# Optimization experiments

Hardware: AMD Instinct MI355X
Metric: run time of the kernel (lower is better)

Reference implementation:

```python
import jax, jax.numpy as jnp
import numpy as np

B, T, D, H = 4, 4096, 2048, 128

def setup_inputs() -> dict:
    key = jax.random.key(0)
    k1, k2, k3, k4 = jax.random.split(key, 4)
    scale = 0.02
    return {
        "x": jax.random.normal(k1, (B, T, D), dtype=jnp.float32),
        "Wq": jax.random.normal(k2, (D, H), dtype=jnp.float32) * scale,
        "Wk": jax.random.normal(k3, (D, H), dtype=jnp.float32) * scale,
        "Wv": jax.random.normal(k4, (D, H), dtype=jnp.float32) * scale,
    }

def reference(x, Wq, Wk, Wv):
    # x: [B,T,D]; projections to [B,T,H]
    q = jnp.einsum('btd,dh->bth', x, Wq)
    k = jnp.einsum('btd,dh->bth', x, Wk)
    v = jnp.einsum('btd,dh->bth', x, Wv)
    scale = 1.0 / jnp.sqrt(jnp.asarray(q.shape[-1], q.dtype))
    scores = jnp.einsum('bth,bsh->bts', q, k) * scale  # [B,T,T]
    t = x.shape[1]
    causal = jnp.tril(jnp.ones((t, t), dtype=bool))
    scores = jnp.where(causal, scores, -jnp.inf)
    weights = jax.nn.softmax(scores, axis=-1)
    # dropout p=0.0 (eval) -> identity
    out = jnp.einsum('bts,bsh->bth', weights, v)
    return out
```

## Files before the change

### kernel.cpp

```cpp
#include <hip/hip_runtime.h>
#include <hip/hip_bf16.h>

#define Bq 4
#define Tq 4096
#define Dq 2048
#define Hq 128
#define Mq (Bq*Tq)
#define CHUNK 16

typedef __attribute__((ext_vector_type(8))) short bf16x8;
typedef __attribute__((ext_vector_type(4))) float f32x4;

static __device__ __forceinline__ short bfbits(float f) {
    union { __hip_bfloat16 h; short s; } u;
    u.h = __float2bfloat16(f);
    return u.s;
}
static __device__ __forceinline__ float bf2f(short s) {
    union { unsigned u; float f; } v;
    v.u = ((unsigned)(unsigned short)s) << 16;
    return v.f;
}

__global__ __launch_bounds__(256, 1) void wt_kernel(
    const float* __restrict__ Wqp,
    const float* __restrict__ Wkp,
    const float* __restrict__ Wvp,
    short* __restrict__ wTg)
{
    __shared__ short trsp[128][136];
    const int kc = blockIdx.x;
    const int w  = blockIdx.y;
    const float* __restrict__ W = (w == 0) ? Wqp : (w == 1) ? Wkp : Wvp;
    const float scale = (w == 0) ? 0.08838834764831843f : 1.0f;
    const int t = threadIdx.x;

    #pragma unroll
    for (int i = 0; i < 16; i++) {
        int idx = t + i * 256;
        int r = idx >> 5, c4 = idx & 31;
        float4 f = *(const float4*)&W[(size_t)(kc * 128 + r) * Hq + c4 * 4];
        trsp[c4 * 4 + 0][r] = bfbits(f.x * scale);
        trsp[c4 * 4 + 1][r] = bfbits(f.y * scale);
        trsp[c4 * 4 + 2][r] = bfbits(f.z * scale);
        trsp[c4 * 4 + 3][r] = bfbits(f.w * scale);
    }
    __syncthreads();
    #pragma unroll
    for (int i = 0; i < 8; i++) {
        int idx = t + i * 256;
        int h = idx >> 4, c8 = idx & 15;
        *(bf16x8*)&wTg[((size_t)w * 128 + h) * Dq + kc * 128 + c8 * 8] =
            *(bf16x8*)&trsp[h][c8 * 8];
    }
}

__global__ __launch_bounds__(256, 1) void qkv_fused_kernel(
    const float* __restrict__ x,
    const short* __restrict__ wTg,
    short* __restrict__ qg,
    short* __restrict__ kg,
    short* __restrict__ vTt)
{
    __shared__ short smem[64 * 72 + 384 * 72];
    short (*xs)[72]  = (short(*)[72])smem;
    short (*wts)[72] = (short(*)[72])(smem + 64 * 72);

    const int m0 = blockIdx.x * 64;

    const int t    = threadIdx.x;
    const int lane = t & 63;
    const int qw   = t >> 6;
    const int l15  = lane & 15;
    const int quad = lane >> 4;

    f32x4 o[4][6];
    #pragma unroll
    for (int mf = 0; mf < 4; mf++)
        #pragma unroll
        for (int j = 0; j < 6; j++) o[mf][j] = (f32x4){0.f, 0.f, 0.f, 0.f};

    const int xr = t >> 2, xc = (t & 3) * 16;

    float4 xreg[4];
    bf16x8 wreg[12];
    {
        const float* src = x + (size_t)(m0 + xr) * Dq + xc;
        #pragma unroll
        for (int i = 0; i < 4; i++) xreg[i] = *(const float4*)(src + i * 4);
        #pragma unroll
        for (int i = 0; i < 12; i++) {
            int idx = t + i * 256;
            wreg[i] = *(const bf16x8*)&wTg[(size_t)(idx >> 3) * Dq + (idx & 7) * 8];
        }
    }

    for (int k0 = 0; k0 < Dq; k0 += 64) {
        __syncthreads();
        {
            bf16x8 v0, v1;
            v0[0] = bfbits(xreg[0].x); v0[1] = bfbits(xreg[0].y);
            v0[2] = bfbits(xreg[0].z); v0[3] = bfbits(xreg[0].w);
            v0[4] = bfbits(xreg[1].x); v0[5] = bfbits(xreg[1].y);
            v0[6] = bfbits(xreg[1].z); v0[7] = bfbits(xreg[1].w);
            v1[0] = bfbits(xreg[2].x); v1[1] = bfbits(xreg[2].y);
            v1[2] = bfbits(xreg[2].z); v1[3] = bfbits(xreg[2].w);
            v1[4] = bfbits(xreg[3].x); v1[5] = bfbits(xreg[3].y);
            v1[6] = bfbits(xreg[3].z); v1[7] = bfbits(xreg[3].w);
            *(bf16x8*)&xs[xr][xc]     = v0;
            *(bf16x8*)&xs[xr][xc + 8] = v1;
            #pragma unroll
            for (int i = 0; i < 12; i++) {
                int idx = t + i * 256;
                *(bf16x8*)&wts[idx >> 3][(idx & 7) * 8] = wreg[i];
            }
        }
        if (k0 + 64 < Dq) {
            const float* src = x + (size_t)(m0 + xr) * Dq + k0 + 64 + xc;
            #pragma unroll
            for (int i = 0; i < 4; i++) xreg[i] = *(const float4*)(src + i * 4);
            #pragma unroll
            for (int i = 0; i < 12; i++) {
                int idx = t + i * 256;
                wreg[i] = *(const bf16x8*)&wTg[(size_t)(idx >> 3) * Dq + k0 + 64 + (idx & 7) * 8];
            }
        }
        __syncthreads();

        #pragma unroll
        for (int kk = 0; kk < 2; kk++) {
            bf16x8 a[4], b[6];
            #pragma unroll
            for (int mf = 0; mf < 4; mf++)
                a[mf] = *(bf16x8*)&xs[mf * 16 + l15][kk * 32 + quad * 8];
            #pragma unroll
            for (int j = 0; j < 6; j++)
                b[j] = *(bf16x8*)&wts[(qw * 6 + j) * 16 + l15][kk * 32 + quad * 8];
            #pragma unroll
            for (int mf = 0; mf < 4; mf++)
                #pragma unroll
                for (int j = 0; j < 6; j++)
                    o[mf][j] = __builtin_amdgcn_mfma_f32_16x16x32_bf16(
                        a[mf], b[j], o[mf][j], 0, 0, 0);
        }
    }

    __syncthreads();
    {
        short (*e64)[264] = (short(*)[264])smem;
        #pragma unroll
        for (int mf = 0; mf < 4; mf++)
            #pragma unroll
            for (int j = 0; j < 6; j++) {
                int n0 = (qw * 6 + j) * 16;
                if (n0 < 256) {
                    #pragma unroll
                    for (int reg = 0; reg < 4; reg++)
                        e64[mf * 16 + quad * 4 + reg][n0 + l15] = bfbits(o[mf][j][reg]);
                }
            }
        __syncthreads();
        #pragma unroll
        for (int i = 0; i < 8; i++) {
            int idx = t + i * 256;
            int r = idx >> 5, u = idx & 31;
            int n = u * 8;
            bf16x8 val = *(bf16x8*)&e64[r][n];
            short* dst = (n < 128) ? &qg[(size_t)(m0 + r) * Hq + n]
                                   : &kg[(size_t)(m0 + r) * Hq + (n - 128)];
            *(bf16x8*)dst = val;
        }
    }
    __syncthreads();
    {
        short (*e128)[72] = (short(*)[72])smem;
        #pragma unroll
        for (int mf = 0; mf < 4; mf++)
            #pragma unroll
            for (int j = 0; j < 6; j++) {
                int n0 = (qw * 6 + j) * 16;
                if (n0 >= 256) {
                    short4 pk;
                    pk.x = bfbits(o[mf][j][0]); pk.y = bfbits(o[mf][j][1]);
                    pk.z = bfbits(o[mf][j][2]); pk.w = bfbits(o[mf][j][3]);
                    *(short4*)&e128[(n0 - 256) + l15][mf * 16 + quad * 4] = pk;
                }
            }
        __syncthreads();
        const int bb = m0 / Tq;
        const int jt = (m0 % Tq) >> 6;
        #pragma unroll
        for (int i = 0; i < 4; i++) {
            int idx = t + i * 256;
            int h = idx >> 3, u = idx & 7;
            *(bf16x8*)&vTt[(((size_t)bb * (Tq / 64) + jt) * 128 + h) * 64 + u * 8] =
                *(bf16x8*)&e128[h][u * 8];
        }
    }
}

__global__ __launch_bounds__(256, 2) void attn_part_kernel(
    const short* __restrict__ qg, const short* __restrict__ kg,
    const short* __restrict__ vTt,
    short* __restrict__ Opart,
    float2* __restrict__ ml)
{
    __shared__ short qs[64][136];
    __shared__ short ks[64][136];
    __shared__ short vt[128][72];
    __shared__ short ps[64][72];

    const int qt = blockIdx.x;
    const int b  = blockIdx.y;
    const int c  = blockIdx.z;
    const int q0 = qt * 64;

    const int lo = c * CHUNK;
    const int hi = min(qt + 1, lo + CHUNK);
    if (lo >= hi) return;

    const int t    = threadIdx.x;
    const int lane = t & 63;
    const int qw   = t >> 6;
    const int l15  = lane & 15;
    const int quad = lane >> 4;

    const size_t zoff = (size_t)c * Mq;

    #pragma unroll
    for (int i = 0; i < 4; i++) {
        int idx = t + i * 256;
        int r = idx >> 4, cc = idx & 15;
        *(bf16x8*)&qs[r][cc * 8] =
            *(const bf16x8*)&qg[(size_t)(b * Tq + q0 + r) * Hq + cc * 8];
    }

    float mcur[4], lrow[4];
    #pragma unroll
    for (int r = 0; r < 4; r++) { mcur[r] = -1e30f; lrow[r] = 0.f; }
    f32x4 o[8];
    #pragma unroll
    for (int nf = 0; nf < 8; nf++) o[nf] = (f32x4){0.f, 0.f, 0.f, 0.f};

    bf16x8 kreg[4], vreg[4];
    {
        const size_t kbase = (size_t)(b * Tq + lo * 64) * Hq;
        const short* vsrc = vTt + (((size_t)b * (Tq / 64) + lo) * 128) * 64;
        #pragma unroll
        for (int i = 0; i < 4; i++) {
            int idx = t + i * 256;
            kreg[i] = *(const bf16x8*)&kg[kbase + (size_t)(idx >> 4) * Hq + (idx & 15) * 8];
            vreg[i] = *(const bf16x8*)&vsrc[idx * 8];
        }
    }

    for (int jt = lo; jt < hi; jt++) {
        __syncthreads();

        #pragma unroll
        for (int i = 0; i < 4; i++) {
            int idx = t + i * 256;
            *(bf16x8*)&ks[idx >> 4][(idx & 15) * 8] = kreg[i];
            *(bf16x8*)&vt[idx >> 3][(idx & 7) * 8]  = vreg[i];
        }
        if (jt + 1 < hi) {
            const size_t kbase = (size_t)(b * Tq + (jt + 1) * 64) * Hq;
            const short* vsrc = vTt + (((size_t)b * (Tq / 64) + jt + 1) * 128) * 64;
            #pragma unroll
            for (int i = 0; i < 4; i++) {
                int idx = t + i * 256;
                kreg[i] = *(const bf16x8*)&kg[kbase + (size_t)(idx >> 4) * Hq + (idx & 15) * 8];
                vreg[i] = *(const bf16x8*)&vsrc[idx * 8];
            }
        }
        __syncthreads();

        f32x4 sacc[4];
        #pragma unroll
        for (int nf = 0; nf < 4; nf++) sacc[nf] = (f32x4){0.f, 0.f, 0.f, 0.f};
        #pragma unroll
        for (int kk = 0; kk < 4; kk++) {
            bf16x8 aq = *(bf16x8*)&qs[qw * 16 + l15][kk * 32 + quad * 8];
            #pragma unroll
            for (int nf = 0; nf < 4; nf++) {
                bf16x8 bk = *(bf16x8*)&ks[nf * 16 + l15][kk * 32 + quad * 8];
                sacc[nf] = __builtin_amdgcn_mfma_f32_16x16x32_bf16(aq, bk, sacc[nf], 0, 0, 0);
            }
        }

        const bool diag = (jt == qt);
        #pragma unroll
        for (int reg = 0; reg < 4; reg++) {
            const int rloc = qw * 16 + quad * 4 + reg;
            if (diag) {
                #pragma unroll
                for (int nf = 0; nf < 4; nf++)
                    if (nf * 16 + l15 > rloc) sacc[nf][reg] = -1e30f;
            }
            float m_r = fmaxf(fmaxf(sacc[0][reg], sacc[1][reg]),
                              fmaxf(sacc[2][reg], sacc[3][reg]));
            #pragma unroll
            for (int mm = 8; mm >= 1; mm >>= 1)
                m_r = fmaxf(m_r, __shfl_xor(m_r, mm, 16));
            float mnew  = fmaxf(mcur[reg], m_r);
            float alpha = __expf(mcur[reg] - mnew);
            mcur[reg]   = mnew;
            float rs = 0.f;
            #pragma unroll
            for (int nf = 0; nf < 4; nf++) {
                float p = __expf(sacc[nf][reg] - mnew);
                rs += p;
                ps[rloc][nf * 16 + l15] = bfbits(p);
            }
            #pragma unroll
            for (int mm = 8; mm >= 1; mm >>= 1)
                rs += __shfl_xor(rs, mm, 16);
            lrow[reg] = lrow[reg] * alpha + rs;
            #pragma unroll
            for (int nf = 0; nf < 8; nf++) o[nf][reg] *= alpha;
        }
        __threadfence_block();

        #pragma unroll
        for (int ks2 = 0; ks2 < 2; ks2++) {
            bf16x8 ap = *(bf16x8*)&ps[qw * 16 + l15][ks2 * 32 + quad * 8];
            #pragma unroll
            for (int nf = 0; nf < 8; nf++) {
                bf16x8 bv = *(bf16x8*)&vt[nf * 16 + l15][ks2 * 32 + quad * 8];
                o[nf] = __builtin_amdgcn_mfma_f32_16x16x32_bf16(ap, bv, o[nf], 0, 0, 0);
            }
        }
    }

    __syncthreads();
    #pragma unroll
    for (int nf = 0; nf < 8; nf++)
        #pragma unroll
        for (int reg = 0; reg < 4; reg++)
            ks[qw * 16 + quad * 4 + reg][nf * 16 + l15] = bfbits(o[nf][reg]);
    if (l15 == 0) {
        #pragma unroll
        for (int reg = 0; reg < 4; reg++)
            ml[zoff + (size_t)b * Tq + q0 + qw * 16 + quad * 4 + reg] =
                make_float2(mcur[reg], lrow[reg]);
    }
    __syncthreads();
    #pragma unroll
    for (int i = 0; i < 4; i++) {
        int idx = t + i * 256;
        int r = idx >> 4, cc = idx & 15;
        *(bf16x8*)&Opart[(zoff + (size_t)b * Tq + q0 + r) * Hq + cc * 8] =
            *(bf16x8*)&ks[r][cc * 8];
    }
}

__global__ __launch_bounds__(256, 4) void merge_kernel(
    const short* __restrict__ Opart, const float2* __restrict__ ml,
    float* __restrict__ outg)
{
    const int t   = threadIdx.x;
    const int row = blockIdx.x * 16 + (t >> 4);
    const int cu  = t & 15;

    const int rl  = row & (Tq - 1);
    const int nch = (rl >> 10) + 1;

    float m = ml[row].x;
    for (int cc = 1; cc < nch; cc++) m = fmaxf(m, ml[(size_t)cc * Mq + row].x);

    float lsum = 0.f;
    float acc[8] = {};
    for (int cc = 0; cc < nch; cc++) {
        float2 p = ml[(size_t)cc * Mq + row];
        float a = __expf(p.x - m);
        lsum += a * p.y;
        bf16x8 oc = *(const bf16x8*)&Opart[((size_t)cc * Mq + row) * Hq + cu * 8];
        #pragma unroll
        for (int j = 0; j < 8; j++) acc[j] += a * bf2f(oc[j]);
    }
    float inv = 1.0f / lsum;

    float4 r0, r1;
    r0.x = acc[0] * inv; r0.y = acc[1] * inv; r0.z = acc[2] * inv; r0.w = acc[3] * inv;
    r1.x = acc[4] * inv; r1.y = acc[5] * inv; r1.z = acc[6] * inv; r1.w = acc[7] * inv;
    float* dst = &outg[(size_t)row * Hq + cu * 8];
    *(float4*)dst       = r0;
    *(float4*)(dst + 4) = r1;
}

extern "C" void kernel_launch(void* const* d_in, const int* in_sizes, int n_in,
                              void* d_out, int out_size, void* d_ws, size_t ws_size,
                              hipStream_t stream) {
    const float* x   = (const float*)d_in[0];
    const float* Wqp = (const float*)d_in[1];
    const float* Wkp = (const float*)d_in[2];
    const float* Wvp = (const float*)d_in[3];
    float* out = (float*)d_out;

    short* qg    = (short*)d_ws;
    short* kg    = qg  + (size_t)Mq * Hq;
    short* vTt   = kg  + (size_t)Mq * Hq;
    short* Opart = vTt + (size_t)Mq * Hq;
    short* wTg   = Opart;
    float2* ml   = (float2*)(Opart + (size_t)4 * Mq * Hq);

    wt_kernel<<<dim3(16, 3), dim3(256), 0, stream>>>(Wqp, Wkp, Wvp, wTg);
    qkv_fused_kernel<<<dim3(Mq / 64), dim3(256), 0, stream>>>(x, wTg, qg, kg, vTt);
    attn_part_kernel<<<dim3(Tq / 64, Bq, 4), dim3(256), 0, stream>>>(qg, kg, vTt, Opart, ml);
    merge_kernel<<<dim3(Mq / 16), dim3(256), 0, stream>>>(Opart, ml, out);
}
```

Baseline: 319.1 us.

## Load K and V MFMA operands directly from global, drop LDS staging and barriers

The attention kernel no longer stages K and V tiles through shared memory with a register prefetch and two block barriers per key tile. Each wave now loads its MFMA B-operands straight from global memory (relying on L1/L2 since all four waves read the same tile). Shared memory shrinks to Q and P, so occupancy is raised from 2 to 4 blocks per CU. The trade-off is that K and V are fetched once per wave instead of once per block, the explicit prefetch of the next tile is gone, and global load latency now sits directly in front of the MFMAs.

```diff
diff --git a/kernel.cpp b/kernel.cpp
--- a/kernel.cpp
+++ b/kernel.cpp
@@ -199,16 +199,15 @@
     }
 }
 
-__global__ __launch_bounds__(256, 2) void attn_part_kernel(
+__global__ __launch_bounds__(256, 4) void attn_part_kernel(
     const short* __restrict__ qg, const short* __restrict__ kg,
     const short* __restrict__ vTt,
     short* __restrict__ Opart,
     float2* __restrict__ ml)
 {
-    __shared__ short qs[64][136];
-    __shared__ short ks[64][136];
-    __shared__ short vt[128][72];
-    __shared__ short ps[64][72];
+    __shared__ short smem[64 * 136 + 64 * 72];
+    short (*qs)[136] = (short(*)[136])smem;
+    short (*ps)[72]  = (short(*)[72])(smem + 64 * 136);
 
     const int qt = blockIdx.x;
     const int b  = blockIdx.y;
@@ -225,12 +224,10 @@
     const int l15  = lane & 15;
     const int quad = lane >> 4;
 
-    const size_t zoff = (size_t)c * Mq;
-
     #pragma unroll
     for (int i = 0; i < 4; i++) {
-        int idx = t + i * 256;
-        int r = idx >> 4, cc = idx & 15;
+        int idx = lane + i * 64;
+        int r = qw * 16 + (idx >> 4), cc = idx & 15;
         *(bf16x8*)&qs[r][cc * 8] =
             *(const bf16x8*)&qg[(size_t)(b * Tq + q0 + r) * Hq + cc * 8];
     }
@@ -242,50 +239,26 @@
     #pragma unroll
     for (int nf = 0; nf < 8; nf++) o[nf] = (f32x4){0.f, 0.f, 0.f, 0.f};
 
-    bf16x8 kreg[4], vreg[4];
-    {
-        const size_t kbase = (size_t)(b * Tq + lo * 64) * Hq;
-        const short* vsrc = vTt + (((size_t)b * (Tq / 64) + lo) * 128) * 64;
-        #pragma unroll
-        for (int i = 0; i < 4; i++) {
-            int idx = t + i * 256;
-            kreg[i] = *(const bf16x8*)&kg[kbase + (size_t)(idx >> 4) * Hq + (idx & 15) * 8];
-            vreg[i] = *(const bf16x8*)&vsrc[idx * 8];
-        }
-    }
+    const short* kptr = kg  + ((size_t)b * Tq + l15) * Hq + quad * 8;
+    const short* vptr = vTt + ((size_t)b * (Tq / 64) * 128 + l15) * 64 + quad * 8;
 
     for (int jt = lo; jt < hi; jt++) {
-        __syncthreads();
-
-        #pragma unroll
-        for (int i = 0; i < 4; i++) {
-            int idx = t + i * 256;
-            *(bf16x8*)&ks[idx >> 4][(idx & 15) * 8] = kreg[i];
-            *(bf16x8*)&vt[idx >> 3][(idx & 7) * 8]  = vreg[i];
-        }
-        if (jt + 1 < hi) {
-            const size_t kbase = (size_t)(b * Tq + (jt + 1) * 64) * Hq;
-            const short* vsrc = vTt + (((size_t)b * (Tq / 64) + jt + 1) * 128) * 64;
-            #pragma unroll
-            for (int i = 0; i < 4; i++) {
-                int idx = t + i * 256;
-                kreg[i] = *(const bf16x8*)&kg[kbase + (size_t)(idx >> 4) * Hq + (idx & 15) * 8];
-                vreg[i] = *(const bf16x8*)&vsrc[idx * 8];
-            }
-        }
-        __syncthreads();
+        const short* kjt = kptr + (size_t)jt * 64 * Hq;
+        const short* vjt = vptr + (size_t)jt * 128 * 64;
 
         f32x4 sacc[4];
         #pragma unroll
         for (int nf = 0; nf < 4; nf++) sacc[nf] = (f32x4){0.f, 0.f, 0.f, 0.f};
         #pragma unroll
         for (int kk = 0; kk < 4; kk++) {
+            bf16x8 bk[4];
+            #pragma unroll
+            for (int nf = 0; nf < 4; nf++)
+                bk[nf] = *(const bf16x8*)(kjt + (size_t)nf * 16 * Hq + kk * 32);
             bf16x8 aq = *(bf16x8*)&qs[qw * 16 + l15][kk * 32 + quad * 8];
             #pragma unroll
-            for (int nf = 0; nf < 4; nf++) {
-                bf16x8 bk = *(bf16x8*)&ks[nf * 16 + l15][kk * 32 + quad * 8];
-                sacc[nf] = __builtin_amdgcn_mfma_f32_16x16x32_bf16(aq, bk, sacc[nf], 0, 0, 0);
-            }
+            for (int nf = 0; nf < 4; nf++)
+                sacc[nf] = __builtin_amdgcn_mfma_f32_16x16x32_bf16(aq, bk[nf], sacc[nf], 0, 0, 0);
         }
 
         const bool diag = (jt == qt);
@@ -323,34 +296,39 @@
 
         #pragma unroll
         for (int ks2 = 0; ks2 < 2; ks2++) {
+            bf16x8 bv[8];
+            #pragma unroll
+            for (int nf = 0; nf < 8; nf++)
+                bv[nf] = *(const bf16x8*)(vjt + (size_t)nf * 16 * 64 + ks2 * 32);
             bf16x8 ap = *(bf16x8*)&ps[qw * 16 + l15][ks2 * 32 + quad * 8];
             #pragma unroll
-            for (int nf = 0; nf < 8; nf++) {
-                bf16x8 bv = *(bf16x8*)&vt[nf * 16 + l15][ks2 * 32 + quad * 8];
-                o[nf] = __builtin_amdgcn_mfma_f32_16x16x32_bf16(ap, bv, o[nf], 0, 0, 0);
-            }
-        }
-    }
-
-    __syncthreads();
-    #pragma unroll
-    for (int nf = 0; nf < 8; nf++)
-        #pragma unroll
-        for (int reg = 0; reg < 4; reg++)
-            ks[qw * 16 + quad * 4 + reg][nf * 16 + l15] = bfbits(o[nf][reg]);
+            for (int nf = 0; nf < 8; nf++)
+                o[nf] = __builtin_amdgcn_mfma_f32_16x16x32_bf16(ap, bv[nf], o[nf], 0, 0, 0);
+        }
+    }
+
+    const size_t zoff = (size_t)c * Mq;
     if (l15 == 0) {
         #pragma unroll
         for (int reg = 0; reg < 4; reg++)
             ml[zoff + (size_t)b * Tq + q0 + qw * 16 + quad * 4 + reg] =
                 make_float2(mcur[reg], lrow[reg]);
     }
+
+    __syncthreads();
+    short (*epi)[136] = (short(*)[136])smem;
+    #pragma unroll
+    for (int nf = 0; nf < 8; nf++)
+        #pragma unroll
+        for (int reg = 0; reg < 4; reg++)
+            epi[qw * 16 + quad * 4 + reg][nf * 16 + l15] = bfbits(o[nf][reg]);
     __syncthreads();
     #pragma unroll
     for (int i = 0; i < 4; i++) {
         int idx = t + i * 256;
         int r = idx >> 4, cc = idx & 15;
         *(bf16x8*)&Opart[(zoff + (size_t)b * Tq + q0 + r) * Hq + cc * 8] =
-            *(bf16x8*)&ks[r][cc * 8];
+            *(bf16x8*)&epi[r][cc * 8];
     }
 }
 
```

After: 457.2 us. 43.3% more time.
